# Performance work log

Measured on AMD Instinct MI355X. Metric: run time of the kernel, lower is better.

Reference implementation:

```python
import jax, jax.numpy as jnp
import numpy as np

N = 8192       # nodes
F = 256        # features
RATIO = 0.5    # fraction of nodes kept
K_KEEP = int(np.ceil(RATIO * N))  # 4096, static for jit
EDGE_PROB = 0.004  # sparse binary adjacency density


def setup_inputs() -> dict:
    key = jax.random.key(0)
    kx, ka, kp = jax.random.split(key, 3)
    X = jax.random.normal(kx, (N, F), dtype=jnp.float32)
    # binary adjacency, ~EDGE_PROB density (layer treats it as dense float)
    A = (jax.random.uniform(ka, (N, N)) < EDGE_PROB).astype(jnp.float32)
    p = jax.random.normal(kp, (F, 1), dtype=jnp.float32)  # learnable kernel
    return {"X": X, "A": A, "p": p}


def reference(X, A, p):
    # y = X p / ||p||  (scores), shape (N, 1)
    p_norm = p / jnp.sqrt(jnp.sum(p * p))
    y = X @ p_norm
    scores = y[:, 0]
    # top-K node indices; boolean_mask in the original preserves original
    # node order, so sort the indices ascending
    _, idx = jax.lax.top_k(scores, K_KEEP)
    idx = jnp.sort(idx)
    # gated features: X * tanh(y), then gather kept rows
    feats = X * jnp.tanh(y)            # (N, F)
    X_pooled = feats[idx]              # (K_KEEP, F)
    # A' = A[idx, idx]
    A_pooled = A[idx][:, idx]          # (K_KEEP, K_KEEP)
    return X_pooled, A_pooled
```

## Files before the change

### kernel.cpp

```cpp
#include <hip/hip_runtime.h>
#include <math.h>

#define N_ROWS 8192
#define F_DIM  256
#define K_KEEP 4096
#define JCH    512

__global__ void k_scores(const float* __restrict__ X, const float* __restrict__ p,
                         float* __restrict__ s_out, float* __restrict__ t_out,
                         int* __restrict__ rank_arr) {
    const int tid  = threadIdx.x;
    const int wv   = tid >> 6;
    const int lane = tid & 63;
    const int row  = blockIdx.x * 4 + wv;

    const int gid = blockIdx.x * 256 + tid;
    if (gid < N_ROWS) rank_arr[gid] = 0;

    const float4 pv = ((const float4*)p)[lane];
    const float4 xv = ((const float4*)(X + (size_t)row * F_DIM))[lane];

    double d  = (double)xv.x * pv.x + (double)xv.y * pv.y
              + (double)xv.z * pv.z + (double)xv.w * pv.w;
    double pp = (double)pv.x * pv.x + (double)pv.y * pv.y
              + (double)pv.z * pv.z + (double)pv.w * pv.w;

    #pragma unroll
    for (int off = 32; off > 0; off >>= 1) {
        d  += __shfl_down(d, off);
        pp += __shfl_down(pp, off);
    }
    if (lane == 0) {
        double y = d / sqrt(pp);
        s_out[row] = (float)y;
        t_out[row] = tanhf((float)y);
    }
}

__global__ void k_rank(const float* __restrict__ s, int* __restrict__ rank_arr) {
    const int ib = blockIdx.x >> 4;
    const int jc = blockIdx.x & 15;
    __shared__ float sk[JCH];
    const int tid = threadIdx.x;

    #pragma unroll
    for (int k = tid; k < JCH; k += 256) sk[k] = s[jc * JCH + k];
    __syncthreads();

    const int   i     = ib * 256 + tid;
    const float si    = s[i];
    const int   jbase = jc * JCH;
    int cnt = 0;
    #pragma unroll 8
    for (int j = 0; j < JCH; ++j) {
        const float v = sk[j];
        cnt += (v > si) ? 1 : 0;
        cnt += ((v == si) && ((jbase + j) < i)) ? 1 : 0;
    }
    atomicAdd(&rank_arr[i], cnt);
}

__global__ void k_compact(const int* __restrict__ rank_arr, int* __restrict__ idx) {
    const int tid  = threadIdx.x;
    const int lane = tid & 63;
    const int wv   = tid >> 6;
    const int base = tid * 32;

    int c = 0;
    #pragma unroll
    for (int k = 0; k < 32; ++k) c += (rank_arr[base + k] < K_KEEP) ? 1 : 0;

    int v = c;
    #pragma unroll
    for (int off = 1; off < 64; off <<= 1) {
        int n = __shfl_up(v, off);
        if (lane >= off) v += n;
    }
    __shared__ int wsum[4];
    if (lane == 63) wsum[wv] = v;
    __syncthreads();
    int wbase = 0;
    for (int w = 0; w < wv; ++w) wbase += wsum[w];

    int pos = wbase + v - c;
    for (int k = 0; k < 32; ++k) {
        const int i = base + k;
        if (rank_arr[i] < K_KEEP) idx[pos++] = i;
    }
}

__global__ void k_xpool(const float* __restrict__ X, const float* __restrict__ t,
                        const int* __restrict__ idx, float* __restrict__ out0) {
    const int tid  = threadIdx.x;
    const int wv   = tid >> 6;
    const int lane = tid & 63;
    const int r    = blockIdx.x * 4 + wv;
    const int src  = idx[r];
    const float tt = t[src];
    float4 v = ((const float4*)X)[(size_t)src * (F_DIM / 4) + lane];
    float4 o = make_float4(v.x * tt, v.y * tt, v.z * tt, v.w * tt);
    ((float4*)out0)[(size_t)r * (F_DIM / 4) + lane] = o;
}

__global__ void k_apool(const float* __restrict__ A, const int* __restrict__ idx,
                        float* __restrict__ out1) {
    const int tid = threadIdx.x;
    const int bx  = blockIdx.x;
    const int r   = bx >> 2;
    const int seg = bx & 3;
    const int src = idx[r];
    const float* Arow = A + (size_t)src * N_ROWS;

    const int4 ci = ((const int4*)idx)[seg * 256 + tid];
    float4 o;
    o.x = Arow[ci.x];
    o.y = Arow[ci.y];
    o.z = Arow[ci.z];
    o.w = Arow[ci.w];
    ((float4*)out1)[(size_t)r * (K_KEEP / 4) + seg * 256 + tid] = o;
}

extern "C" void kernel_launch(void* const* d_in, const int* in_sizes, int n_in,
                              void* d_out, int out_size, void* d_ws, size_t ws_size,
                              hipStream_t stream) {
    const float* X = (const float*)d_in[0];
    const float* A = (const float*)d_in[1];
    const float* p = (const float*)d_in[2];

    float* ws_f   = (float*)d_ws;
    float* s_arr  = ws_f;
    float* t_arr  = ws_f + N_ROWS;
    int*   rank_a = (int*)(ws_f + 2 * N_ROWS);
    int*   idx    = (int*)(ws_f + 3 * N_ROWS);

    float* out0 = (float*)d_out;
    float* out1 = out0 + (size_t)K_KEEP * F_DIM;

    k_scores <<<N_ROWS / 4, 256, 0, stream>>>(X, p, s_arr, t_arr, rank_a);
    k_rank   <<<32 * 16,    256, 0, stream>>>(s_arr, rank_a);
    k_compact<<<1,          256, 0, stream>>>(rank_a, idx);
    k_xpool  <<<K_KEEP / 4, 256, 0, stream>>>(X, t_arr, idx, out0);
    k_apool  <<<K_KEEP * 4, 256, 0, stream>>>(A, idx, out1);
}
```

Baseline: 382.0 us.

## Fuse pooling kernels and stage adjacency rows in shared memory before gathering

Merges the feature and adjacency pooling kernels into one launch with one block per kept row. Each block loads the full selected adjacency row with coalesced float4 reads into shared memory, then gathers the kept columns from LDS instead of issuing scattered global loads. This trades per-element random global accesses for a contiguous row read, at the cost of 32KB of LDS per block limiting occupancy and reading unused columns.

Result: no change. 381.4 us (-0.2%).

```diff
diff --git a/kernel.cpp b/kernel.cpp
--- a/kernel.cpp
+++ b/kernel.cpp
@@ -89,35 +89,44 @@
     }
 }
 
-__global__ void k_xpool(const float* __restrict__ X, const float* __restrict__ t,
-                        const int* __restrict__ idx, float* __restrict__ out0) {
-    const int tid  = threadIdx.x;
-    const int wv   = tid >> 6;
-    const int lane = tid & 63;
-    const int r    = blockIdx.x * 4 + wv;
-    const int src  = idx[r];
+__global__ __launch_bounds__(256) void k_pool(const float* __restrict__ X,
+                                              const float* __restrict__ A,
+                                              const float* __restrict__ t,
+                                              const int* __restrict__ idx,
+                                              float* __restrict__ out0,
+                                              float* __restrict__ out1) {
+    __shared__ float row[N_ROWS];
+    const int tid = threadIdx.x;
+    const int r   = blockIdx.x;
+    const int src = idx[r];
+
+    const float4* Arow4 = (const float4*)(A + (size_t)src * N_ROWS);
+    float4 tmp[8];
+    #pragma unroll
+    for (int k = 0; k < 8; ++k) tmp[k] = Arow4[k * 256 + tid];
+    #pragma unroll
+    for (int k = 0; k < 8; ++k) ((float4*)row)[k * 256 + tid] = tmp[k];
+
     const float tt = t[src];
-    float4 v = ((const float4*)X)[(size_t)src * (F_DIM / 4) + lane];
-    float4 o = make_float4(v.x * tt, v.y * tt, v.z * tt, v.w * tt);
-    ((float4*)out0)[(size_t)r * (F_DIM / 4) + lane] = o;
-}
+    if (tid < 64) {
+        float4 v = ((const float4*)(X + (size_t)src * F_DIM))[tid];
+        ((float4*)(out0 + (size_t)r * F_DIM))[tid] =
+            make_float4(v.x * tt, v.y * tt, v.z * tt, v.w * tt);
+    }
+    __syncthreads();
 
-__global__ void k_apool(const float* __restrict__ A, const int* __restrict__ idx,
-                        float* __restrict__ out1) {
-    const int tid = threadIdx.x;
-    const int bx  = blockIdx.x;
-    const int r   = bx >> 2;
-    const int seg = bx & 3;
-    const int src = idx[r];
-    const float* Arow = A + (size_t)src * N_ROWS;
-
-    const int4 ci = ((const int4*)idx)[seg * 256 + tid];
-    float4 o;
-    o.x = Arow[ci.x];
-    o.y = Arow[ci.y];
-    o.z = Arow[ci.z];
-    o.w = Arow[ci.w];
-    ((float4*)out1)[(size_t)r * (K_KEEP / 4) + seg * 256 + tid] = o;
+    const int4* idx4 = (const int4*)idx;
+    float4* o4 = (float4*)(out1 + (size_t)r * K_KEEP);
+    #pragma unroll
+    for (int k = 0; k < 4; ++k) {
+        const int4 ci = idx4[k * 256 + tid];
+        float4 o;
+        o.x = row[ci.x];
+        o.y = row[ci.y];
+        o.z = row[ci.z];
+        o.w = row[ci.w];
+        o4[k * 256 + tid] = o;
+    }
 }
 
 extern "C" void kernel_launch(void* const* d_in, const int* in_sizes, int n_in,
@@ -139,6 +148,5 @@
     k_scores <<<N_ROWS / 4, 256, 0, stream>>>(X, p, s_arr, t_arr, rank_a);
     k_rank   <<<32 * 16,    256, 0, stream>>>(s_arr, rank_a);
     k_compact<<<1,          256, 0, stream>>>(rank_a, idx);
-    k_xpool  <<<K_KEEP / 4, 256, 0, stream>>>(X, t_arr, idx, out0);
-    k_apool  <<<K_KEEP * 4, 256, 0, stream>>>(A, idx, out1);
+    k_pool   <<<K_KEEP,     256, 0, stream>>>(X, A, t_arr, idx, out0, out1);
 }
```
